# Optimization experiments

Measured on AMD Instinct MI355X. Metric: run time of the kernel, lower is better.

Reference implementation:

```python
import jax, jax.numpy as jnp
from jax import lax
import numpy as np

D_MODEL = 1024
EXPAND = 2
D_INNER = D_MODEL * EXPAND
D_STATE = 16
D_CONV = 4
DECAY = 0.95
LN_EPS = 1e-5


def setup_inputs() -> dict:
    key = jax.random.key(0)
    ks = jax.random.split(key, 9)
    b, s = 4, 2048
    scale = 1.0 / np.sqrt(D_MODEL)
    inner_scale = 1.0 / np.sqrt(D_INNER)
    return {
        "x": jax.random.normal(ks[0], (b, s, D_MODEL), dtype=jnp.float32),
        "W_in": jax.random.normal(ks[1], (2 * D_INNER, D_MODEL), dtype=jnp.float32) * scale,
        "conv_w": jax.random.normal(ks[2], (D_INNER, 1, D_CONV), dtype=jnp.float32) * 0.5,
        "conv_b": jax.random.normal(ks[3], (D_INNER,), dtype=jnp.float32) * 0.1,
        "W_x": jax.random.normal(ks[4], (2 * D_STATE, D_INNER), dtype=jnp.float32) * inner_scale,
        "B_log": jax.random.normal(ks[5], (D_INNER, D_STATE), dtype=jnp.float32) * 0.05,  # xavier-ish small
        "W_out": jax.random.normal(ks[6], (D_MODEL, D_INNER), dtype=jnp.float32) * inner_scale,
        "ln_g": jnp.ones((D_MODEL,), dtype=jnp.float32),
        "ln_b": jnp.zeros((D_MODEL,), dtype=jnp.float32),
    }


def _ssm_block(x, W_in, conv_w, conv_b, W_x, B_log, W_out, ln_g, ln_b):
    b, s, _ = x.shape
    d_inner = W_in.shape[0] // 2
    d_conv = conv_w.shape[-1]

    # input projection and gate split
    xz = jnp.einsum('bsd,ed->bse', x, W_in)            # [b, s, 2*d_inner]
    x_inner, z = jnp.split(xz, 2, axis=-1)             # each [b, s, d_inner]

    # causal depthwise conv (left pad d_conv-1, output length s)
    xc = jnp.transpose(x_inner, (0, 2, 1))             # [b, d_inner, s]
    conv = lax.conv_general_dilated(
        xc, conv_w, window_strides=(1,), padding=[(d_conv - 1, 0)],
        feature_group_count=d_inner)
    conv = conv + conv_b[None, :, None]
    x_conv = jax.nn.silu(jnp.transpose(conv, (0, 2, 1)))  # [b, s, d_inner]

    # selective parameters; s_B is produced but unused in the original math
    sp = jnp.einsum('bsd,nd->bsn', x_conv, W_x)        # [b, s, 2*d_state]
    _s_B, s_C = jnp.split(sp, 2, axis=-1)              # each [b, s, d_state]

    B = jnp.exp(B_log)                                  # [d_inner, d_state]

    # state_t = 0.95*state_{t-1} + B * x_t  factorizes as  state = B[d,n]*h[b,t,d]
    # with h_t = 0.95*h_{t-1} + x_conv_t ; scan over time with [b, d_inner] carry.
    def step(h, xt):
        h = DECAY * h + xt
        return h, h

    h0 = jnp.zeros((b, d_inner), dtype=x.dtype)
    _, h = lax.scan(step, h0, jnp.swapaxes(x_conv, 0, 1))  # [s, b, d_inner]
    h = jnp.swapaxes(h, 0, 1)                              # [b, s, d_inner]

    # output_t[b,d] = sum_n state[b,d,n]*s_C[b,t,n] = h[b,t,d] * (s_C @ B^T)[b,t,d]
    y = h * jnp.einsum('bsn,dn->bsd', s_C, B)
    y = y * jax.nn.silu(z)
    y = jnp.einsum('bsd,od->bso', y, W_out)            # [b, s, d_model]

    resid = x + y
    mu = jnp.mean(resid, axis=-1, keepdims=True)
    var = jnp.var(resid, axis=-1, keepdims=True)
    return (resid - mu) * lax.rsqrt(var + LN_EPS) * ln_g + ln_b


def reference(x, W_in, conv_w, conv_b, W_x, B_log, W_out, ln_g, ln_b):
    return _ssm_block(x, W_in, conv_w, conv_b, W_x, B_log, W_out, ln_g, ln_b)
```

## Files before the change

### kernel.cpp

```cpp
#include <hip/hip_runtime.h>
#include <hip/hip_bf16.h>
#include <stdint.h>

#define DM   1024
#define DI   2048
#define NST  16
#define BSZ  4
#define SLEN 2048
#define MROWS (BSZ*SLEN)
#define CHUNK 8
#define NCH  (SLEN/CHUNK)
#define DECAYF 0.95f
#define MB (size_t)1048576

typedef _Float16 f16;
typedef __attribute__((ext_vector_type(2))) _Float16 f16x2;
typedef __attribute__((ext_vector_type(4))) _Float16 f16x4;
typedef __attribute__((ext_vector_type(8))) _Float16 f16x8;
typedef __attribute__((ext_vector_type(4))) float f32x4;

__device__ __forceinline__ float silu_f(float v) { return v / (1.f + __expf(-v)); }

__device__ __forceinline__ void gload16(const f16* lds, const f16* g) {
  __builtin_amdgcn_global_load_lds((const __attribute__((address_space(1))) void*)g,
                                   (__attribute__((address_space(3))) void*)lds, 16, 0, 0);
}

#define NX4  (MROWS * DM / 4)
#define NWI4 (2 * DI * DM / 4)
#define NWO4 (DM * DI / 4)
#define NWX4 (NST * DI / 4)
#define NE4  (NST * DI / 4)
__global__ __launch_bounds__(256) void cvt_all(
    const float* __restrict__ x, const float* __restrict__ wi, const float* __restrict__ wo,
    const float* __restrict__ Wx, const float* __restrict__ B_log,
    f16* __restrict__ A1, f16* __restrict__ B1, f16* __restrict__ W2,
    f16* __restrict__ WxC, f16* __restrict__ expBT)
{
  int i = blockIdx.x * 256 + threadIdx.x;
  if (i < NX4 + NWI4 + NWO4 + NWX4) {
    const float* src; f16* dst; int j;
    if (i < NX4)                     { src = x;  dst = A1; j = i; }
    else if (i < NX4 + NWI4)         { src = wi; dst = B1; j = i - NX4; }
    else if (i < NX4 + NWI4 + NWO4)  { src = wo; dst = W2; j = i - NX4 - NWI4; }
    else                             { src = Wx + (size_t)NST * DI; dst = WxC; j = i - NX4 - NWI4 - NWO4; }
    float4 v = ((const float4*)src)[j];
    f16x4 o = {(f16)v.x, (f16)v.y, (f16)v.z, (f16)v.w};
    ((f16x4*)dst)[j] = o;
  } else {
    int j = i - NX4 - NWI4 - NWO4 - NWX4;
    int base = j * 4;
    int n = base >> 11, d = base & (DI - 1);
    f16x4 o = {(f16)__expf(B_log[(d + 0) * NST + n]), (f16)__expf(B_log[(d + 1) * NST + n]),
               (f16)__expf(B_log[(d + 2) * NST + n]), (f16)__expf(B_log[(d + 3) * NST + n])};
    ((f16x4*)expBT)[j] = o;
  }
}

template<int MODE>
__global__ __launch_bounds__(256) void gemm_bt(
    const f16* __restrict__ A, const f16* __restrict__ Bt,
    int K, f16* __restrict__ O0, f16* __restrict__ O1)
{
  __shared__ __align__(16) f16 sA[128 * 64];
  __shared__ __align__(16) f16 sB[128 * 64];
  const int tid  = threadIdx.x;
  const int lane = tid & 63;
  const int w    = tid >> 6;
  const int wr   = w >> 1, wc = w & 1;

  const int nwg  = gridDim.x * gridDim.y;
  int wgid = blockIdx.y * gridDim.x + blockIdx.x;
  wgid = (wgid & 7) * (nwg >> 3) + (wgid >> 3);
  const int bx = wgid % gridDim.x;
  const int by = wgid / gridDim.x;

  const int mBase = by * 128;
  const int nBase = bx * 128;
  const int lr = lane & 15;
  const int lu = lane >> 4;

  f32x4 acc[4][4];
  #pragma unroll
  for (int m = 0; m < 4; ++m)
    #pragma unroll
    for (int n = 0; n < 4; ++n)
      acc[m][n] = (f32x4){0.f, 0.f, 0.f, 0.f};

  int offA[4][2], offB[4][2];
  #pragma unroll
  for (int m = 0; m < 4; ++m) {
    int ra = wr * 64 + m * 16 + lr;
    int rb = wc * 64 + m * 16 + lr;
    #pragma unroll
    for (int kk = 0; kk < 2; ++kk) {
      offA[m][kk] = ra * 64 + ((kk * 4 + lu) ^ (ra & 7)) * 8;
      offB[m][kk] = rb * 64 + ((kk * 4 + lu) ^ (rb & 7)) * 8;
    }
  }

  for (int k0 = 0; k0 < K; k0 += 64) {
    #pragma unroll
    for (int j = 0; j < 4; ++j) {
      int c = j * 256 + tid;
      int row = c >> 3, p = c & 7;
      int su = p ^ (row & 7);
      gload16(&sA[c * 8], A  + (size_t)(mBase + row) * K + k0 + su * 8);
      gload16(&sB[c * 8], Bt + (size_t)(nBase + row) * K + k0 + su * 8);
    }
    __syncthreads();
    #pragma unroll
    for (int kk = 0; kk < 2; ++kk) {
      f16x8 af[4], bf[4];
      #pragma unroll
      for (int m = 0; m < 4; ++m) af[m] = *(const f16x8*)&sA[offA[m][kk]];
      #pragma unroll
      for (int n = 0; n < 4; ++n) bf[n] = *(const f16x8*)&sB[offB[n][kk]];
      #pragma unroll
      for (int m = 0; m < 4; ++m)
        #pragma unroll
        for (int n = 0; n < 4; ++n)
          acc[m][n] = __builtin_amdgcn_mfma_f32_16x16x32_f16(af[m], bf[n], acc[m][n], 0, 0, 0);
    }
    __syncthreads();
  }

  const int rq = (lane >> 4) * 4;
  f16* sOut = sA;
  const bool isZ = (MODE == 1) && (nBase >= DI);
  f16* dst = (MODE == 0) ? O0 : (isZ ? O1 : O0);
  const int ncols = (MODE == 0) ? DM : DI;
  const int cb = isZ ? (nBase - DI) : nBase;
  #pragma unroll
  for (int m = 0; m < 4; ++m) {
    #pragma unroll
    for (int n = 0; n < 4; ++n)
      #pragma unroll
      for (int r = 0; r < 4; ++r)
        sOut[(wr * 16 + rq + r) * 128 + wc * 64 + n * 16 + lr] = (f16)acc[m][n][r];
    __syncthreads();
    #pragma unroll
    for (int q = 0; q < 2; ++q) {
      int cidx = q * 256 + tid;
      int orow = cidx >> 4;
      int ocol = (cidx & 15) * 8;
      int grow = mBase + (orow >> 4) * 64 + m * 16 + (orow & 15);
      f16x8 v = *(const f16x8*)&sOut[orow * 128 + ocol];
      *(f16x8*)&dst[(size_t)grow * ncols + cb + ocol] = v;
    }
    __syncthreads();
  }
}

__global__ __launch_bounds__(256) void conv_scan(
    const f16* __restrict__ Xi, const float* __restrict__ convW, const float* __restrict__ convB,
    f16* __restrict__ Xc, f16* __restrict__ Hl, float* __restrict__ L)
{
  const int tid = threadIdx.x;
  const int d0 = tid * 8;
  const int ch = blockIdx.x;
  const int b  = blockIdx.y;
  const int t0 = ch * CHUNK;

  float w0[8], w1[8], w2[8], w3[8], cb[8];
  #pragma unroll
  for (int i = 0; i < 8; ++i) {
    float4 wv = ((const float4*)convW)[d0 + i];
    w0[i] = wv.x; w1[i] = wv.y; w2[i] = wv.z; w3[i] = wv.w;
    cb[i] = convB[d0 + i];
  }

  float xm3[8], xm2[8], xm1[8];
  auto loadrow = [&](int t, float* dst) {
    if (t < 0) {
      #pragma unroll
      for (int i = 0; i < 8; ++i) dst[i] = 0.f;
      return;
    }
    f16x8 v = *(const f16x8*)&Xi[((size_t)(b * SLEN + t)) * DI + d0];
    #pragma unroll
    for (int i = 0; i < 8; ++i) dst[i] = (float)v[i];
  };
  loadrow(t0 - 3, xm3); loadrow(t0 - 2, xm2); loadrow(t0 - 1, xm1);

  float h[8] = {0.f, 0.f, 0.f, 0.f, 0.f, 0.f, 0.f, 0.f};
  for (int t = 0; t < CHUNK; ++t) {
    const size_t ro = ((size_t)(b * SLEN + t0 + t)) * DI + d0;
    f16x8 xv = *(const f16x8*)&Xi[ro];
    f16x8 xco, hho;
    #pragma unroll
    for (int i = 0; i < 8; ++i) {
      float xt = (float)xv[i];
      float c = cb[i] + w0[i]*xm3[i] + w1[i]*xm2[i] + w2[i]*xm1[i] + w3[i]*xt;
      float xc = silu_f(c);
      h[i] = DECAYF * h[i] + xc;
      xco[i] = (f16)xc;
      hho[i] = (f16)h[i];
      xm3[i] = xm2[i]; xm2[i] = xm1[i]; xm1[i] = xt;
    }
    *(f16x8*)&Xc[ro] = xco;
    *(f16x8*)&Hl[ro] = hho;
  }
  const size_t lo = ((size_t)(b * NCH + ch)) * DI + d0;
  float4 l0 = {h[0], h[1], h[2], h[3]};
  float4 l1 = {h[4], h[5], h[6], h[7]};
  *(float4*)&L[lo] = l0;
  *(float4*)&L[lo + 4] = l1;
}

__global__ void carry_scan(const float* __restrict__ L, f16* __restrict__ Carry) {
  int i = blockIdx.x * blockDim.x + threadIdx.x;
  int b = i >> 11, d = i & (DI - 1);
  float dp = 1.f;
  #pragma unroll
  for (int k = 0; k < CHUNK; ++k) dp *= DECAYF;
  float c = 0.f;
  for (int ch0 = 0; ch0 < NCH; ch0 += 8) {
    float lv[8];
    #pragma unroll
    for (int k = 0; k < 8; ++k)
      lv[k] = L[((size_t)(b * NCH + ch0 + k)) * DI + d];
    #pragma unroll
    for (int k = 0; k < 8; ++k) {
      c = dp * c + lv[k];
      Carry[((size_t)(b * NCH + ch0 + k)) * DI + d] = (f16)c;
    }
  }
}

__global__ __launch_bounds__(256) void sc_gemm(const f16* __restrict__ Xc, const f16* __restrict__ WxC,
                                               float* __restrict__ sC) {
  const int m = blockIdx.x * 4 + (threadIdx.x >> 6);
  const int lane = threadIdx.x & 63;
  float acc[16];
  #pragma unroll
  for (int n = 0; n < 16; ++n) acc[n] = 0.f;
  #pragma unroll
  for (int it = 0; it < DI / 512; ++it) {
    int d = it * 512 + lane * 8;
    f16x8 xv = *(const f16x8*)&Xc[(size_t)m * DI + d];
    #pragma unroll
    for (int n = 0; n < 16; ++n) {
      f16x8 wv = *(const f16x8*)&WxC[(size_t)n * DI + d];
      float s = 0.f;
      #pragma unroll
      for (int i = 0; i < 8; ++i) s += (float)xv[i] * (float)wv[i];
      acc[n] += s;
    }
  }
  #pragma unroll
  for (int n = 0; n < 16; ++n) {
    #pragma unroll
    for (int off = 32; off > 0; off >>= 1) acc[n] += __shfl_xor(acc[n], off);
  }
  if (lane == 0) {
    #pragma unroll
    for (int n = 0; n < 16; ++n) sC[m * 16 + n] = acc[n];
  }
}

__global__ __launch_bounds__(256) void ew_y(
    const f16* __restrict__ Hl, const f16* __restrict__ Zs,
    const float* __restrict__ sC, const f16* __restrict__ expBT,
    const f16* __restrict__ Carry, f16* __restrict__ Y)
{
  const int r = threadIdx.x >> 6, lane = threadIdx.x & 63;
  const int m = blockIdx.y * 4 + r;
  const int d0 = blockIdx.x * 512 + lane * 8;
  const int b = m >> 11, t = m & (SLEN - 1);
  const int ch = t / CHUNK, tl = t & (CHUNK - 1);

  float coef = 0.f;
  if (ch > 0) {
    coef = 1.f;
    for (int j = 0; j <= tl; ++j) coef *= DECAYF;
  }

  const float4 sc0 = *(const float4*)&sC[m * 16 + 0];
  const float4 sc1 = *(const float4*)&sC[m * 16 + 4];
  const float4 sc2 = *(const float4*)&sC[m * 16 + 8];
  const float4 sc3 = *(const float4*)&sC[m * 16 + 12];
  const float scv[16] = {sc0.x, sc0.y, sc0.z, sc0.w, sc1.x, sc1.y, sc1.z, sc1.w,
                         sc2.x, sc2.y, sc2.z, sc2.w, sc3.x, sc3.y, sc3.z, sc3.w};

  const size_t ro = (size_t)m * DI + d0;
  f16x8 hvv = *(const f16x8*)&Hl[ro];
  f16x8 zvv = *(const f16x8*)&Zs[ro];
  float hv[8], zv[8], ca[8];
  #pragma unroll
  for (int i = 0; i < 8; ++i) {
    hv[i] = (float)hvv[i];
    zv[i] = silu_f((float)zvv[i]);
    ca[i] = 0.f;
  }
  if (ch > 0) {
    const size_t co = ((size_t)(b * NCH + ch - 1)) * DI + d0;
    f16x8 cv = *(const f16x8*)&Carry[co];
    #pragma unroll
    for (int i = 0; i < 8; ++i) ca[i] = (float)cv[i];
  }

  float cp[8] = {0.f, 0.f, 0.f, 0.f, 0.f, 0.f, 0.f, 0.f};
  #pragma unroll
  for (int n = 0; n < 16; ++n) {
    f16x8 ev = *(const f16x8*)&expBT[(size_t)n * DI + d0];
    #pragma unroll
    for (int i = 0; i < 8; ++i) cp[i] += scv[n] * (float)ev[i];
  }

  f16x8 o;
  #pragma unroll
  for (int i = 0; i < 8; ++i) {
    float y = (hv[i] + coef * ca[i]) * cp[i] * zv[i];
    o[i] = (f16)y;
  }
  *(f16x8*)&Y[ro] = o;
}

__global__ __launch_bounds__(256) void ln_res(const f16* __restrict__ G, const float* __restrict__ x,
                                              const float* __restrict__ lng, const float* __restrict__ lnb,
                                              float* __restrict__ out) {
  const int m = blockIdx.x;
  const int tid = threadIdx.x;
  f16x4 gv4 = ((const f16x4*)(G + (size_t)m * DM))[tid];
  float4 xv = ((const float4*)(x + (size_t)m * DM))[tid];
  float4 rv = {(float)gv4.x + xv.x, (float)gv4.y + xv.y, (float)gv4.z + xv.z, (float)gv4.w + xv.w};
  float s = rv.x + rv.y + rv.z + rv.w;
  float s2 = rv.x * rv.x + rv.y * rv.y + rv.z * rv.z + rv.w * rv.w;
  #pragma unroll
  for (int off = 32; off > 0; off >>= 1) {
    s += __shfl_xor(s, off);
    s2 += __shfl_xor(s2, off);
  }
  __shared__ float ps[8];
  const int w = tid >> 6;
  if ((tid & 63) == 0) { ps[w] = s; ps[w + 4] = s2; }
  __syncthreads();
  float S = ps[0] + ps[1] + ps[2] + ps[3];
  float S2 = ps[4] + ps[5] + ps[6] + ps[7];
  float mu = S * (1.f / DM);
  float var = S2 * (1.f / DM) - mu * mu;
  float rs = rsqrtf(var + 1e-5f);
  float4 gg = ((const float4*)lng)[tid];
  float4 bb = ((const float4*)lnb)[tid];
  float4 ov = {(rv.x - mu) * rs * gg.x + bb.x, (rv.y - mu) * rs * gg.y + bb.y,
               (rv.z - mu) * rs * gg.z + bb.z, (rv.w - mu) * rs * gg.w + bb.w};
  ((float4*)(out + (size_t)m * DM))[tid] = ov;
}

extern "C" void kernel_launch(void* const* d_in, const int* in_sizes, int n_in,
                              void* d_out, int out_size, void* d_ws, size_t ws_size,
                              hipStream_t stream) {
  const float* x      = (const float*)d_in[0];
  const float* W_in   = (const float*)d_in[1];
  const float* conv_w = (const float*)d_in[2];
  const float* conv_b = (const float*)d_in[3];
  const float* W_x    = (const float*)d_in[4];
  const float* B_log  = (const float*)d_in[5];
  const float* W_out  = (const float*)d_in[6];
  const float* ln_g   = (const float*)d_in[7];
  const float* ln_b   = (const float*)d_in[8];
  float* out = (float*)d_out;

  char* ws = (char*)d_ws;
  f16*   Xi  = (f16*)(ws + 0);
  f16*   Yp  = (f16*)(ws + 0);
  f16*   Zs  = (f16*)(ws + 32 * MB);
  f16*   Xc  = (f16*)(ws + 64 * MB);
  f16*   Hl  = (f16*)(ws + 96 * MB);
  f16*   A1  = (f16*)(ws + 128 * MB);
  f16*   B1  = (f16*)(ws + 144 * MB);
  f16*   W2  = (f16*)(ws + 152 * MB);
  f16*   G   = (f16*)(ws + 156 * MB);
  float* L     = (float*)(ws + 172 * MB);
  f16*   Carry = (f16*)(ws + 180 * MB);
  float* sC    = (float*)(ws + 184 * MB);
  f16*   expBT = (f16*)(ws + 185 * MB);
  f16*   WxC   = (f16*)(ws + 186 * MB);

  cvt_all<<<(NX4 + NWI4 + NWO4 + NWX4 + NE4) / 256, 256, 0, stream>>>(
      x, W_in, W_out, W_x, B_log, A1, B1, W2, WxC, expBT);

  gemm_bt<1><<<dim3(2 * DI / 128, MROWS / 128), 256, 0, stream>>>(A1, B1, DM, Xi, Zs);

  conv_scan<<<dim3(NCH, BSZ), 256, 0, stream>>>(Xi, conv_w, conv_b, Xc, Hl, L);
  carry_scan<<<(BSZ * DI) / 256, 256, 0, stream>>>(L, Carry);
  sc_gemm<<<MROWS / 4, 256, 0, stream>>>(Xc, WxC, sC);
  ew_y<<<dim3(DI / 512, MROWS / 4), 256, 0, stream>>>(Hl, Zs, sC, expBT, Carry, Yp);

  gemm_bt<0><<<dim3(DM / 128, MROWS / 128), 256, 0, stream>>>(Yp, W2, DI, G, nullptr);

  ln_res<<<MROWS, 256, 0, stream>>>(G, x, ln_g, ln_b, out);
}
```

Baseline: 266.0 us.

## Lengthen scan chunks, fuse carry scan with LDS-staged s_C projection

```diff
diff --git a/kernel.cpp b/kernel.cpp
--- a/kernel.cpp
+++ b/kernel.cpp
@@ -8,7 +8,7 @@
 #define BSZ  4
 #define SLEN 2048
 #define MROWS (BSZ*SLEN)
-#define CHUNK 8
+#define CHUNK 32
 #define NCH  (SLEN/CHUNK)
 #define DECAYF 0.95f
 #define MB (size_t)1048576
@@ -157,39 +157,39 @@
     f16* __restrict__ Xc, f16* __restrict__ Hl, float* __restrict__ L)
 {
   const int tid = threadIdx.x;
-  const int d0 = tid * 8;
-  const int ch = blockIdx.x;
-  const int b  = blockIdx.y;
+  const int d0 = (blockIdx.x * 256 + tid) * 4;
+  const int ch = blockIdx.y;
+  const int b  = blockIdx.z;
   const int t0 = ch * CHUNK;
 
-  float w0[8], w1[8], w2[8], w3[8], cb[8];
-  #pragma unroll
-  for (int i = 0; i < 8; ++i) {
+  float w0[4], w1[4], w2[4], w3[4], cb[4];
+  #pragma unroll
+  for (int i = 0; i < 4; ++i) {
     float4 wv = ((const float4*)convW)[d0 + i];
     w0[i] = wv.x; w1[i] = wv.y; w2[i] = wv.z; w3[i] = wv.w;
     cb[i] = convB[d0 + i];
   }
 
-  float xm3[8], xm2[8], xm1[8];
+  float xm3[4], xm2[4], xm1[4];
   auto loadrow = [&](int t, float* dst) {
     if (t < 0) {
       #pragma unroll
-      for (int i = 0; i < 8; ++i) dst[i] = 0.f;
+      for (int i = 0; i < 4; ++i) dst[i] = 0.f;
       return;
     }
-    f16x8 v = *(const f16x8*)&Xi[((size_t)(b * SLEN + t)) * DI + d0];
-    #pragma unroll
-    for (int i = 0; i < 8; ++i) dst[i] = (float)v[i];
+    f16x4 v = *(const f16x4*)&Xi[((size_t)(b * SLEN + t)) * DI + d0];
+    #pragma unroll
+    for (int i = 0; i < 4; ++i) dst[i] = (float)v[i];
   };
   loadrow(t0 - 3, xm3); loadrow(t0 - 2, xm2); loadrow(t0 - 1, xm1);
 
-  float h[8] = {0.f, 0.f, 0.f, 0.f, 0.f, 0.f, 0.f, 0.f};
+  float h[4] = {0.f, 0.f, 0.f, 0.f};
   for (int t = 0; t < CHUNK; ++t) {
     const size_t ro = ((size_t)(b * SLEN + t0 + t)) * DI + d0;
-    f16x8 xv = *(const f16x8*)&Xi[ro];
-    f16x8 xco, hho;
-    #pragma unroll
-    for (int i = 0; i < 8; ++i) {
+    f16x4 xv = *(const f16x4*)&Xi[ro];
+    f16x4 xco, hho;
+    #pragma unroll
+    for (int i = 0; i < 4; ++i) {
       float xt = (float)xv[i];
       float c = cb[i] + w0[i]*xm3[i] + w1[i]*xm2[i] + w2[i]*xm1[i] + w3[i]*xt;
       float xc = silu_f(c);
@@ -198,64 +198,85 @@
       hho[i] = (f16)h[i];
       xm3[i] = xm2[i]; xm2[i] = xm1[i]; xm1[i] = xt;
     }
-    *(f16x8*)&Xc[ro] = xco;
-    *(f16x8*)&Hl[ro] = hho;
+    *(f16x4*)&Xc[ro] = xco;
+    *(f16x4*)&Hl[ro] = hho;
   }
   const size_t lo = ((size_t)(b * NCH + ch)) * DI + d0;
   float4 l0 = {h[0], h[1], h[2], h[3]};
-  float4 l1 = {h[4], h[5], h[6], h[7]};
   *(float4*)&L[lo] = l0;
-  *(float4*)&L[lo + 4] = l1;
-}
-
-__global__ void carry_scan(const float* __restrict__ L, f16* __restrict__ Carry) {
-  int i = blockIdx.x * blockDim.x + threadIdx.x;
-  int b = i >> 11, d = i & (DI - 1);
-  float dp = 1.f;
-  #pragma unroll
-  for (int k = 0; k < CHUNK; ++k) dp *= DECAYF;
-  float c = 0.f;
-  for (int ch0 = 0; ch0 < NCH; ch0 += 8) {
-    float lv[8];
-    #pragma unroll
-    for (int k = 0; k < 8; ++k)
-      lv[k] = L[((size_t)(b * NCH + ch0 + k)) * DI + d];
-    #pragma unroll
-    for (int k = 0; k < 8; ++k) {
-      c = dp * c + lv[k];
-      Carry[((size_t)(b * NCH + ch0 + k)) * DI + d] = (f16)c;
-    }
-  }
-}
-
-__global__ __launch_bounds__(256) void sc_gemm(const f16* __restrict__ Xc, const f16* __restrict__ WxC,
-                                               float* __restrict__ sC) {
-  const int m = blockIdx.x * 4 + (threadIdx.x >> 6);
-  const int lane = threadIdx.x & 63;
-  float acc[16];
-  #pragma unroll
-  for (int n = 0; n < 16; ++n) acc[n] = 0.f;
-  #pragma unroll
-  for (int it = 0; it < DI / 512; ++it) {
-    int d = it * 512 + lane * 8;
-    f16x8 xv = *(const f16x8*)&Xc[(size_t)m * DI + d];
+}
+
+__global__ __launch_bounds__(256) void mid_fused(
+    const f16* __restrict__ Xc, const f16* __restrict__ WxC, const float* __restrict__ L,
+    float* __restrict__ sC, f16* __restrict__ Carry)
+{
+  __shared__ __align__(16) f16 sW[16 * 2048];
+  const int tid = threadIdx.x;
+
+  if (blockIdx.x >= 512) {
+    int i = (blockIdx.x - 512) * 256 + tid;
+    int b = i >> 11, d = i & (DI - 1);
+    float dp = 1.f;
+    #pragma unroll
+    for (int k = 0; k < CHUNK; ++k) dp *= DECAYF;
+    float c = 0.f;
+    for (int ch0 = 0; ch0 < NCH; ch0 += 8) {
+      float lv[8];
+      #pragma unroll
+      for (int k = 0; k < 8; ++k)
+        lv[k] = L[((size_t)(b * NCH + ch0 + k)) * DI + d];
+      #pragma unroll
+      for (int k = 0; k < 8; ++k) {
+        c = dp * c + lv[k];
+        Carry[((size_t)(b * NCH + ch0 + k)) * DI + d] = (f16)c;
+      }
+    }
+    return;
+  }
+
+  const int m0 = blockIdx.x * 16;
+  const int w = tid >> 6, lane = tid & 63;
+
+  #pragma unroll
+  for (int j = 0; j < 16; ++j)
+    ((f16x8*)sW)[j * 256 + tid] = ((const f16x8*)WxC)[j * 256 + tid];
+  __syncthreads();
+
+  float acc[4][16];
+  #pragma unroll
+  for (int r = 0; r < 4; ++r)
+    #pragma unroll
+    for (int n = 0; n < 16; ++n) acc[r][n] = 0.f;
+
+  #pragma unroll
+  for (int r = 0; r < 4; ++r) {
+    const int m = m0 + w * 4 + r;
+    #pragma unroll
+    for (int it = 0; it < 4; ++it) {
+      int d = it * 512 + lane * 8;
+      f16x8 xv = *(const f16x8*)&Xc[(size_t)m * DI + d];
+      #pragma unroll
+      for (int n = 0; n < 16; ++n) {
+        f16x8 wv = *(const f16x8*)&sW[n * 2048 + d];
+        float s = 0.f;
+        #pragma unroll
+        for (int i = 0; i < 8; ++i) s += (float)xv[i] * (float)wv[i];
+        acc[r][n] += s;
+      }
+    }
+  }
+
+  #pragma unroll
+  for (int r = 0; r < 4; ++r) {
     #pragma unroll
     for (int n = 0; n < 16; ++n) {
-      f16x8 wv = *(const f16x8*)&WxC[(size_t)n * DI + d];
-      float s = 0.f;
-      #pragma unroll
-      for (int i = 0; i < 8; ++i) s += (float)xv[i] * (float)wv[i];
-      acc[n] += s;
-    }
-  }
-  #pragma unroll
-  for (int n = 0; n < 16; ++n) {
-    #pragma unroll
-    for (int off = 32; off > 0; off >>= 1) acc[n] += __shfl_xor(acc[n], off);
-  }
-  if (lane == 0) {
-    #pragma unroll
-    for (int n = 0; n < 16; ++n) sC[m * 16 + n] = acc[n];
+      #pragma unroll
+      for (int off = 32; off > 0; off >>= 1) acc[r][n] += __shfl_xor(acc[r][n], off);
+    }
+    if (lane == 0) {
+      #pragma unroll
+      for (int n = 0; n < 16; ++n) sC[(m0 + w * 4 + r) * 16 + n] = acc[r][n];
+    }
   }
 }
 
@@ -373,19 +394,18 @@
   f16*   W2  = (f16*)(ws + 152 * MB);
   f16*   G   = (f16*)(ws + 156 * MB);
   float* L     = (float*)(ws + 172 * MB);
-  f16*   Carry = (f16*)(ws + 180 * MB);
-  float* sC    = (float*)(ws + 184 * MB);
-  f16*   expBT = (f16*)(ws + 185 * MB);
-  f16*   WxC   = (f16*)(ws + 186 * MB);
+  f16*   Carry = (f16*)(ws + 174 * MB);
+  float* sC    = (float*)(ws + 175 * MB);
+  f16*   expBT = (f16*)(ws + 176 * MB);
+  f16*   WxC   = (f16*)(ws + 177 * MB);
 
   cvt_all<<<(NX4 + NWI4 + NWO4 + NWX4 + NE4) / 256, 256, 0, stream>>>(
       x, W_in, W_out, W_x, B_log, A1, B1, W2, WxC, expBT);
 
   gemm_bt<1><<<dim3(2 * DI / 128, MROWS / 128), 256, 0, stream>>>(A1, B1, DM, Xi, Zs);
 
-  conv_scan<<<dim3(NCH, BSZ), 256, 0, stream>>>(Xi, conv_w, conv_b, Xc, Hl, L);
-  carry_scan<<<(BSZ * DI) / 256, 256, 0, stream>>>(L, Carry);
-  sc_gemm<<<MROWS / 4, 256, 0, stream>>>(Xc, WxC, sC);
+  conv_scan<<<dim3(DI / 1024, NCH, BSZ), 256, 0, stream>>>(Xi, conv_w, conv_b, Xc, Hl, L);
+  mid_fused<<<544, 256, 0, stream>>>(Xc, WxC, L, sC, Carry);
   ew_y<<<dim3(DI / 512, MROWS / 4), 256, 0, stream>>>(Hl, Zs, sC, expBT, Carry, Yp);
 
   gemm_bt<0><<<dim3(DM / 128, MROWS / 128), 256, 0, stream>>>(Yp, W2, DI, G, nullptr);
```

New measurement: 430.6 us. 61.9% more time.
